# Optimization experiments

Hardware: AMD Instinct MI355X
Metric: run time of the kernel (lower is better)

Reference implementation:

```python
import jax, jax.numpy as jnp
import numpy as np

THRESHOLD = 1e-3  # hardcoded `thresholds = 0.001` in the sparse branch


def setup_inputs() -> dict:
    key = jax.random.key(0)
    k1, k2, k3, k4, k5 = jax.random.split(key, 5)
    b, r, d_in, d_out = 8, 4096, 768, 768
    x = jax.random.normal(k1, (b, r, d_in), dtype=jnp.float32)
    weight = jax.random.normal(k2, (d_out, d_in), dtype=jnp.float32) * 0.02
    bias = jax.random.normal(k3, (d_out,), dtype=jnp.float32) * 0.02
    U = jax.random.normal(k4, (d_in, d_in), dtype=jnp.float32) * (d_in ** -0.5)
    VT = jax.random.normal(k5, (d_out, d_out), dtype=jnp.float32) * (d_out ** -0.5)
    return {"x": x, "weight": weight, "bias": bias, "U": U, "VT": VT}


def reference(x, weight, bias, U, VT):
    # Sparse path (len_grads >= 30) of LinearFunctionSparseGrad.forward.
    # h = x @ U.T, rotated into the gradient basis.  [b, r, c]
    h = jnp.einsum('brc,dc->brd', x, U)
    # Threshold-sparsify: zero entries with |h| <= 0.001.
    h = jnp.where(jnp.abs(h) > THRESHOLD, h, jnp.zeros((), h.dtype))
    # Original: gather nonzero rows/cols, h[rows][:, cols] @ weight.T[cols],
    # then scatter back via I[:, rows] @ res_. Dropped cols are exactly-zero
    # columns and dropped rows are exactly-zero rows, so the math equals a
    # dense matmul on the masked tensor (no [b*r, b*r] identity needed).
    res = jnp.einsum('brc,oc->bro', h, weight)        # h @ weight.T
    res = jnp.einsum('bro,po->brp', res, VT)          # res_ @ VT.T (self.VT=VT_orig.T => VT here)
    return res + bias
```

## Files before the change

### kernel.cpp

```cpp
#include <hip/hip_runtime.h>
#include <hip/hip_bf16.h>

typedef __bf16 bf16_t;
typedef bf16_t bf16x8 __attribute__((ext_vector_type(8)));
typedef bf16_t bf16x4 __attribute__((ext_vector_type(4)));
typedef float  f32x4  __attribute__((ext_vector_type(4)));

#define BM 256
#define BN 256
#define BK 64

enum { EPI_NONE = 0, EPI_THRESH = 1, EPI_BIAS = 2 };

__device__ __forceinline__ void memfence() { asm volatile("" ::: "memory"); }
__device__ __forceinline__ void blockbar() {
    memfence(); __builtin_amdgcn_s_barrier(); memfence();
}

#define GLD16(src, dst) __builtin_amdgcn_global_load_lds( \
    (const __attribute__((address_space(1))) void*)(src), \
    (__attribute__((address_space(3))) void*)(dst), 16, 0, 0)

template <int EPI, typename CT>
__device__ __forceinline__
void gemm_tile(const bf16_t* __restrict__ A, const bf16_t* __restrict__ B,
               CT* __restrict__ C, const float* __restrict__ bias,
               int m0, int n0, int N, int K,
               bf16_t* __restrict__ As, bf16_t* __restrict__ Bs)
{
    const int lane = threadIdx.x & 63;
    const int wave = threadIdx.x >> 6;
    const int wm = wave >> 2;
    const int wn = wave & 3;

    const int fm  = lane & 15;
    const int ql  = lane >> 4;
    const int fsw = fm & 7;

    const int NT = K / BK;

    const int choff = ((lane & 7) ^ ((lane >> 3) & 7)) * 8;
    const bf16_t* pA[2]; const bf16_t* pB[2];
    int sd[2];
#pragma unroll
    for (int l = 0; l < 2; ++l) {
        const int r = (wave * 2 + l) * 8 + (lane >> 3);
        pA[l] = A + (size_t)(m0 + r) * K + choff;
        pB[l] = B + (size_t)(n0 + r) * K + choff;
        sd[l] = (wave * 2 + l) * 64;
    }

#define STAGE_TILE(tt, Ad, Bd) do {                                          \
    _Pragma("unroll") for (int h_ = 0; h_ < 2; ++h_)                         \
    _Pragma("unroll") for (int l_ = 0; l_ < 2; ++l_) {                       \
        GLD16(pA[l_] + (size_t)h_ * 128 * K + (size_t)(tt) * BK,             \
              (Ad) + (size_t)(h_ * 1024 + sd[l_]) * 8);                      \
        GLD16(pB[l_] + (size_t)h_ * 128 * K + (size_t)(tt) * BK,             \
              (Bd) + (size_t)(h_ * 1024 + sd[l_]) * 8);                      \
    } } while (0)

#define LOAD_A(mh) do {                                                      \
    _Pragma("unroll") for (int i_ = 0; i_ < 4; ++i_)                         \
    _Pragma("unroll") for (int k_ = 0; k_ < 2; ++k_)                         \
        af[i_][k_] = *(const bf16x8*)(Ab + (size_t)(                         \
            (wm * 128 + (mh) * 64 + i_ * 16 + fm) * 8 +                      \
            ((k_ * 4 + ql) ^ fsw)) * 8); } while (0)

#define LOAD_B(nh) do {                                                      \
    _Pragma("unroll") for (int j_ = 0; j_ < 2; ++j_)                         \
    _Pragma("unroll") for (int k_ = 0; k_ < 2; ++k_)                         \
        bfx[j_][k_] = *(const bf16x8*)(Bb + (size_t)(                        \
            (wn * 64 + (nh) * 32 + j_ * 16 + fm) * 8 +                       \
            ((k_ * 4 + ql) ^ fsw)) * 8); } while (0)

#define MFMA_Q(mh, nh) do {                                                  \
    _Pragma("unroll") for (int i_ = 0; i_ < 4; ++i_)                         \
    _Pragma("unroll") for (int j_ = 0; j_ < 2; ++j_)                         \
    _Pragma("unroll") for (int k_ = 0; k_ < 2; ++k_)                         \
        acc[(mh) * 4 + i_][(nh) * 2 + j_] =                                  \
            __builtin_amdgcn_mfma_f32_16x16x32_bf16(                         \
                af[i_][k_], bfx[j_][k_],                                     \
                acc[(mh) * 4 + i_][(nh) * 2 + j_], 0, 0, 0); } while (0)

#define PHASE_TAIL(mh, nh) do {                                              \
    blockbar();                                                              \
    asm volatile("s_waitcnt lgkmcnt(0)" ::: "memory");                       \
    __builtin_amdgcn_sched_barrier(0);                                       \
    __builtin_amdgcn_s_setprio(1);                                           \
    MFMA_Q(mh, nh);                                                          \
    __builtin_amdgcn_s_setprio(0);                                           \
    blockbar(); } while (0)

    f32x4 acc[8][4];
#pragma unroll
    for (int i = 0; i < 8; ++i)
#pragma unroll
        for (int j = 0; j < 4; ++j) acc[i][j] = (f32x4){0.f, 0.f, 0.f, 0.f};

    STAGE_TILE(0, As, Bs);
    asm volatile("s_waitcnt vmcnt(0)" ::: "memory");
    blockbar();

    for (int t = 0; t < NT; ++t) {
        const int cur = t & 1;
        const bf16_t* __restrict__ Ab = As + cur * (BM * BK);
        const bf16_t* __restrict__ Bb = Bs + cur * (BN * BK);
        bf16_t* Asd = As + (cur ^ 1) * (BM * BK);
        bf16_t* Bsd = Bs + (cur ^ 1) * (BN * BK);

        bf16x8 af[4][2], bfx[2][2];

        LOAD_A(0); LOAD_B(0);
        if (t + 1 < NT) STAGE_TILE(t + 1, Asd, Bsd);
        PHASE_TAIL(0, 0);

        LOAD_B(1);
        PHASE_TAIL(0, 1);

        LOAD_A(1);
        PHASE_TAIL(1, 1);

        LOAD_B(0);
        asm volatile("s_waitcnt vmcnt(0)" ::: "memory");
        PHASE_TAIL(1, 0);
    }

#pragma unroll
    for (int mi = 0; mi < 8; ++mi) {
#pragma unroll
        for (int ni = 0; ni < 4; ++ni) {
            const int col = n0 + wn * 64 + ni * 16 + fm;
            float bv = 0.f;
            if (EPI == EPI_BIAS) bv = bias[col];
#pragma unroll
            for (int r = 0; r < 4; ++r) {
                const int row = m0 + wm * 128 + mi * 16 + ql * 4 + r;
                float v = acc[mi][ni][r];
                if (EPI == EPI_THRESH) v = (fabsf(v) > 1e-3f) ? v : 0.f;
                if (EPI == EPI_BIAS) v += bv;
                C[(size_t)row * N + col] = (CT)v;
            }
        }
    }

#undef STAGE_TILE
#undef LOAD_A
#undef LOAD_B
#undef MFMA_Q
#undef PHASE_TAIL
}

__global__ __launch_bounds__(512, 2)
void gemm_h_wc(const bf16_t* __restrict__ xb, const bf16_t* __restrict__ Ub,
               bf16_t* __restrict__ h,
               const bf16_t* __restrict__ VTb, const bf16_t* __restrict__ Wt,
               bf16_t* __restrict__ Wc)
{
    __shared__ __align__(16) bf16_t As[2 * BM * BK];
    __shared__ __align__(16) bf16_t Bs[2 * BN * BK];
    const int b = blockIdx.x;
    if (b < 384) {
        const int L = (b & 7) * 48 + (b >> 3);
        gemm_tile<EPI_THRESH, bf16_t>(xb, Ub, h, nullptr,
                                      (L / 3) * BM, (L % 3) * BN, 768, 768, As, Bs);
    } else {
        const int b2 = b - 384;
        gemm_tile<EPI_NONE, bf16_t>(VTb, Wt, Wc, nullptr,
                                    (b2 / 3) * BM, (b2 % 3) * BN, 768, 768, As, Bs);
    }
}

__global__ __launch_bounds__(512, 2)
void gemm_out(const bf16_t* __restrict__ h, const bf16_t* __restrict__ Wc,
              float* __restrict__ out, const float* __restrict__ bias)
{
    __shared__ __align__(16) bf16_t As[2 * BM * BK];
    __shared__ __align__(16) bf16_t Bs[2 * BN * BK];
    const int b = blockIdx.x;
    const int L = (b & 7) * 48 + (b >> 3);
    gemm_tile<EPI_BIAS, float>(h, Wc, out, bias,
                               (L / 3) * BM, (L % 3) * BN, 768, 768, As, Bs);
}

__global__ __launch_bounds__(256)
void prep(const float* __restrict__ x, const float* __restrict__ U,
          const float* __restrict__ VT, const float* __restrict__ w,
          bf16_t* __restrict__ xb, bf16_t* __restrict__ Ub,
          bf16_t* __restrict__ VTb, bf16_t* __restrict__ Wt)
{
    __shared__ float tt[32][33];
    const int b = blockIdx.x;
    if (b < 25728) {
        const float* src; bf16_t* dst; int i;
        if (b < 24576)      { src = x;  dst = xb;  i = b * 256 + threadIdx.x; }
        else if (b < 25152) { src = U;  dst = Ub;  i = (b - 24576) * 256 + threadIdx.x; }
        else                { src = VT; dst = VTb; i = (b - 25152) * 256 + threadIdx.x; }
        const f32x4 v = ((const f32x4*)src)[i];
        bf16x4 o;
        o[0] = (bf16_t)v[0]; o[1] = (bf16_t)v[1];
        o[2] = (bf16_t)v[2]; o[3] = (bf16_t)v[3];
        ((bf16x4*)dst)[i] = o;
    } else {
        const int t = b - 25728;
        const int bx = (t % 24) * 32, by = (t / 24) * 32;
        const int tx = threadIdx.x & 31, ty = threadIdx.x >> 5;
#pragma unroll
        for (int i = 0; i < 32; i += 8)
            tt[ty + i][tx] = w[(size_t)(by + ty + i) * 768 + bx + tx];
        __syncthreads();
#pragma unroll
        for (int i = 0; i < 32; i += 8)
            Wt[(size_t)(bx + ty + i) * 768 + by + tx] = (bf16_t)tt[tx][ty + i];
    }
}

extern "C" void kernel_launch(void* const* d_in, const int* in_sizes, int n_in,
                              void* d_out, int out_size, void* d_ws, size_t ws_size,
                              hipStream_t stream)
{
    const float* x    = (const float*)d_in[0];
    const float* w    = (const float*)d_in[1];
    const float* bias = (const float*)d_in[2];
    const float* U    = (const float*)d_in[3];
    const float* VT   = (const float*)d_in[4];
    float* out = (float*)d_out;

    const int D = 768;
    const int M = 8 * 4096;
    const size_t MD = (size_t)M * D;
    const size_t DD = (size_t)D * D;

    char* ws = (char*)d_ws;
    bf16_t* xb  = (bf16_t*)ws;
    bf16_t* h   = (bf16_t*)(ws + MD * 2);
    bf16_t* Ub  = (bf16_t*)(ws + MD * 4);
    bf16_t* VTb = (bf16_t*)(ws + MD * 4 + DD * 2);
    bf16_t* Wt  = (bf16_t*)(ws + MD * 4 + DD * 4);
    bf16_t* Wc  = (bf16_t*)(ws + MD * 4 + DD * 6);

    prep<<<26304, 256, 0, stream>>>(x, U, VT, w, xb, Ub, VTb, Wt);
    gemm_h_wc<<<384 + 9, 512, 0, stream>>>(xb, Ub, h, VTb, Wt, Wc);
    gemm_out<<<384, 512, 0, stream>>>(h, Wc, out, bias);
}
```

Measured before the change: 299.8 us.

## Fuse fp32-to-bf16 conversion into first GEMM loads, drop prep kernel

Removes the separate prep kernel that converted x, U, VT and transposed W to bf16. The first GEMM now reads fp32 directly through registers, converts to bf16 and writes into swizzled LDS. It uses a new 256x128 tile with double-buffering through registers instead of direct global-to-LDS loads. This avoids writing and re-reading a bf16 copy of x, but it reads fp32 x twice as wide per GEMM pass (once per N tile) and loses the async LDS load path, and the strided W read is uncoalesced.

```diff
diff --git a/kernel.cpp b/kernel.cpp
--- a/kernel.cpp
+++ b/kernel.cpp
@@ -6,8 +6,6 @@
 typedef bf16_t bf16x4 __attribute__((ext_vector_type(4)));
 typedef float  f32x4  __attribute__((ext_vector_type(4)));
 
-#define BM 256
-#define BN 256
 #define BK 64
 
 enum { EPI_NONE = 0, EPI_THRESH = 1, EPI_BIAS = 2 };
@@ -21,12 +19,171 @@
     (const __attribute__((address_space(1))) void*)(src), \
     (__attribute__((address_space(3))) void*)(dst), 16, 0, 0)
 
-template <int EPI, typename CT>
+template <int EPI, int STRIDED_B>
 __device__ __forceinline__
-void gemm_tile(const bf16_t* __restrict__ A, const bf16_t* __restrict__ B,
-               CT* __restrict__ C, const float* __restrict__ bias,
-               int m0, int n0, int N, int K,
-               bf16_t* __restrict__ As, bf16_t* __restrict__ Bs)
+void gemm_h_tile(const float* __restrict__ A, const float* __restrict__ B,
+                 bf16_t* __restrict__ C, int m0, int n0, int N, int K,
+                 bf16_t* __restrict__ As, bf16_t* __restrict__ Bs)
+{
+    const int lane = threadIdx.x & 63;
+    const int wave = threadIdx.x >> 6;
+    const int wm = wave >> 1;
+    const int wn = wave & 1;
+
+    const int fm  = lane & 15;
+    const int ql  = lane >> 4;
+    const int fsw = fm & 7;
+
+    const int NT = K / BK;
+
+    const int arow = wave * 32 + (lane >> 1);
+    const int acb  = (lane & 1) * 4;
+    const float* pa = A + (size_t)(m0 + arow) * K + acb * 8;
+    const int brow = wave * 16 + (lane >> 2);
+    const int bcb  = (lane & 3) * 2;
+    const float* pb = STRIDED_B ? (B + (size_t)(n0 + brow))
+                                : (B + (size_t)(n0 + brow) * K + bcb * 8);
+
+    f32x4 ar[8]; f32x4 brv[4]; float bsv[16];
+
+#define H_ISSUE(tt) do {                                                     \
+    _Pragma("unroll") for (int i_ = 0; i_ < 8; ++i_)                         \
+        ar[i_] = *(const f32x4*)(pa + (size_t)(tt) * BK + i_ * 4);           \
+    if (!STRIDED_B) {                                                        \
+        _Pragma("unroll") for (int i_ = 0; i_ < 4; ++i_)                     \
+            brv[i_] = *(const f32x4*)(pb + (size_t)(tt) * BK + i_ * 4);      \
+    } else {                                                                 \
+        _Pragma("unroll") for (int i_ = 0; i_ < 16; ++i_)                    \
+            bsv[i_] = pb[(size_t)((tt) * BK + bcb * 8 + i_) * K];            \
+    } } while (0)
+
+#define H_WRITE(Ad, Bd) do {                                                 \
+    _Pragma("unroll") for (int c_ = 0; c_ < 4; ++c_) {                       \
+        bf16x8 w_;                                                           \
+        _Pragma("unroll") for (int e_ = 0; e_ < 4; ++e_) {                   \
+            w_[e_]     = (bf16_t)ar[c_ * 2][e_];                             \
+            w_[4 + e_] = (bf16_t)ar[c_ * 2 + 1][e_];                         \
+        }                                                                    \
+        *(bf16x8*)((Ad) + (size_t)(arow * 8 + ((acb + c_) ^ (arow & 7))) * 8)\
+            = w_;                                                            \
+    }                                                                        \
+    _Pragma("unroll") for (int c_ = 0; c_ < 2; ++c_) {                       \
+        bf16x8 w_;                                                           \
+        if (!STRIDED_B) {                                                    \
+            _Pragma("unroll") for (int e_ = 0; e_ < 4; ++e_) {               \
+                w_[e_]     = (bf16_t)brv[c_ * 2][e_];                        \
+                w_[4 + e_] = (bf16_t)brv[c_ * 2 + 1][e_];                    \
+            }                                                                \
+        } else {                                                             \
+            _Pragma("unroll") for (int e_ = 0; e_ < 8; ++e_)                 \
+                w_[e_] = (bf16_t)bsv[c_ * 8 + e_];                           \
+        }                                                                    \
+        *(bf16x8*)((Bd) + (size_t)(brow * 8 + ((bcb + c_) ^ (brow & 7))) * 8)\
+            = w_;                                                            \
+    } } while (0)
+
+    f32x4 acc[4][4];
+#pragma unroll
+    for (int i = 0; i < 4; ++i)
+#pragma unroll
+        for (int j = 0; j < 4; ++j) acc[i][j] = (f32x4){0.f, 0.f, 0.f, 0.f};
+
+    H_ISSUE(0);
+    asm volatile("s_waitcnt vmcnt(0)" ::: "memory");
+    H_WRITE(As, Bs);
+    asm volatile("s_waitcnt lgkmcnt(0)" ::: "memory");
+    blockbar();
+
+    for (int t = 0; t < NT; ++t) {
+        const int cur = t & 1;
+        const bf16_t* __restrict__ Ab = As + cur * (256 * BK);
+        const bf16_t* __restrict__ Bb = Bs + cur * (128 * BK);
+        bf16_t* Asd = As + (cur ^ 1) * (256 * BK);
+        bf16_t* Bsd = Bs + (cur ^ 1) * (128 * BK);
+        const bool stage = (t + 1 < NT);
+
+        bf16x8 af[4][2], bfr[2][2];
+
+        if (stage) H_ISSUE(t + 1);
+#pragma unroll
+        for (int i = 0; i < 4; ++i) {
+            const int row = wm * 64 + i * 16 + fm;
+#pragma unroll
+            for (int kk = 0; kk < 2; ++kk)
+                af[i][kk] = *(const bf16x8*)(Ab + (size_t)(row * 8 + ((kk * 4 + ql) ^ fsw)) * 8);
+        }
+#pragma unroll
+        for (int j = 0; j < 2; ++j) {
+            const int row = wn * 64 + j * 16 + fm;
+#pragma unroll
+            for (int kk = 0; kk < 2; ++kk)
+                bfr[j][kk] = *(const bf16x8*)(Bb + (size_t)(row * 8 + ((kk * 4 + ql) ^ fsw)) * 8);
+        }
+        blockbar();
+        asm volatile("s_waitcnt lgkmcnt(0)" ::: "memory");
+        __builtin_amdgcn_sched_barrier(0);
+        __builtin_amdgcn_s_setprio(1);
+#pragma unroll
+        for (int i = 0; i < 4; ++i)
+#pragma unroll
+            for (int j = 0; j < 2; ++j)
+#pragma unroll
+                for (int kk = 0; kk < 2; ++kk)
+                    acc[i][j] = __builtin_amdgcn_mfma_f32_16x16x32_bf16(
+                        af[i][kk], bfr[j][kk], acc[i][j], 0, 0, 0);
+        __builtin_amdgcn_s_setprio(0);
+        blockbar();
+
+#pragma unroll
+        for (int j = 0; j < 2; ++j) {
+            const int row = wn * 64 + (j + 2) * 16 + fm;
+#pragma unroll
+            for (int kk = 0; kk < 2; ++kk)
+                bfr[j][kk] = *(const bf16x8*)(Bb + (size_t)(row * 8 + ((kk * 4 + ql) ^ fsw)) * 8);
+        }
+        if (stage) {
+            asm volatile("s_waitcnt vmcnt(0)" ::: "memory");
+            H_WRITE(Asd, Bsd);
+        }
+        asm volatile("s_waitcnt lgkmcnt(0)" ::: "memory");
+        blockbar();
+        __builtin_amdgcn_sched_barrier(0);
+        __builtin_amdgcn_s_setprio(1);
+#pragma unroll
+        for (int i = 0; i < 4; ++i)
+#pragma unroll
+            for (int j = 0; j < 2; ++j)
+#pragma unroll
+                for (int kk = 0; kk < 2; ++kk)
+                    acc[i][j + 2] = __builtin_amdgcn_mfma_f32_16x16x32_bf16(
+                        af[i][kk], bfr[j][kk], acc[i][j + 2], 0, 0, 0);
+        __builtin_amdgcn_s_setprio(0);
+        blockbar();
+    }
+
+#pragma unroll
+    for (int i = 0; i < 4; ++i) {
+#pragma unroll
+        for (int j = 0; j < 4; ++j) {
+            const int col = n0 + wn * 64 + j * 16 + fm;
+#pragma unroll
+            for (int r = 0; r < 4; ++r) {
+                const int row = m0 + wm * 64 + i * 16 + ql * 4 + r;
+                float v = acc[i][j][r];
+                if (EPI == EPI_THRESH) v = (fabsf(v) > 1e-3f) ? v : 0.f;
+                C[(size_t)row * N + col] = (bf16_t)v;
+            }
+        }
+    }
+#undef H_ISSUE
+#undef H_WRITE
+}
+
+__device__ __forceinline__
+void gemm_o_tile(const bf16_t* __restrict__ A, const bf16_t* __restrict__ B,
+                 float* __restrict__ C, const float* __restrict__ bias,
+                 int m0, int n0, int N, int K,
+                 bf16_t* __restrict__ As, bf16_t* __restrict__ Bs)
 {
     const int lane = threadIdx.x & 63;
     const int wave = threadIdx.x >> 6;
@@ -103,10 +260,10 @@
 
     for (int t = 0; t < NT; ++t) {
         const int cur = t & 1;
-        const bf16_t* __restrict__ Ab = As + cur * (BM * BK);
-        const bf16_t* __restrict__ Bb = Bs + cur * (BN * BK);
-        bf16_t* Asd = As + (cur ^ 1) * (BM * BK);
-        bf16_t* Bsd = Bs + (cur ^ 1) * (BN * BK);
+        const bf16_t* __restrict__ Ab = As + cur * (256 * BK);
+        const bf16_t* __restrict__ Bb = Bs + cur * (256 * BK);
+        bf16_t* Asd = As + (cur ^ 1) * (256 * BK);
+        bf16_t* Bsd = Bs + (cur ^ 1) * (256 * BK);
 
         bf16x8 af[4][2], bfx[2][2];
 
@@ -130,19 +287,14 @@
 #pragma unroll
         for (int ni = 0; ni < 4; ++ni) {
             const int col = n0 + wn * 64 + ni * 16 + fm;
-            float bv = 0.f;
-            if (EPI == EPI_BIAS) bv = bias[col];
+            const float bv = bias[col];
 #pragma unroll
             for (int r = 0; r < 4; ++r) {
                 const int row = m0 + wm * 128 + mi * 16 + ql * 4 + r;
-                float v = acc[mi][ni][r];
-                if (EPI == EPI_THRESH) v = (fabsf(v) > 1e-3f) ? v : 0.f;
-                if (EPI == EPI_BIAS) v += bv;
-                C[(size_t)row * N + col] = (CT)v;
+                C[(size_t)row * N + col] = acc[mi][ni][r] + bv;
             }
         }
     }
-
 #undef STAGE_TILE
 #undef LOAD_A
 #undef LOAD_B
@@ -151,22 +303,22 @@
 }
 
 __global__ __launch_bounds__(512, 2)
-void gemm_h_wc(const bf16_t* __restrict__ xb, const bf16_t* __restrict__ Ub,
+void gemm_h_wc(const float* __restrict__ x, const float* __restrict__ U,
                bf16_t* __restrict__ h,
-               const bf16_t* __restrict__ VTb, const bf16_t* __restrict__ Wt,
+               const float* __restrict__ VT, const float* __restrict__ w,
                bf16_t* __restrict__ Wc)
 {
-    __shared__ __align__(16) bf16_t As[2 * BM * BK];
-    __shared__ __align__(16) bf16_t Bs[2 * BN * BK];
+    __shared__ __align__(16) bf16_t As[2 * 256 * BK];
+    __shared__ __align__(16) bf16_t Bs[2 * 128 * BK];
     const int b = blockIdx.x;
-    if (b < 384) {
-        const int L = (b & 7) * 48 + (b >> 3);
-        gemm_tile<EPI_THRESH, bf16_t>(xb, Ub, h, nullptr,
-                                      (L / 3) * BM, (L % 3) * BN, 768, 768, As, Bs);
+    if (b < 768) {
+        const int L = (b & 7) * 96 + (b >> 3);
+        gemm_h_tile<EPI_THRESH, 0>(x, U, h,
+                                   (L / 6) * 256, (L % 6) * 128, 768, 768, As, Bs);
     } else {
-        const int b2 = b - 384;
-        gemm_tile<EPI_NONE, bf16_t>(VTb, Wt, Wc, nullptr,
-                                    (b2 / 3) * BM, (b2 % 3) * BN, 768, 768, As, Bs);
+        const int b2 = b - 768;
+        gemm_h_tile<EPI_NONE, 1>(VT, w, Wc,
+                                 (b2 / 6) * 256, (b2 % 6) * 128, 768, 768, As, Bs);
     }
 }
 
@@ -174,44 +326,12 @@
 void gemm_out(const bf16_t* __restrict__ h, const bf16_t* __restrict__ Wc,
               float* __restrict__ out, const float* __restrict__ bias)
 {
-    __shared__ __align__(16) bf16_t As[2 * BM * BK];
-    __shared__ __align__(16) bf16_t Bs[2 * BN * BK];
+    __shared__ __align__(16) bf16_t As[2 * 256 * BK];
+    __shared__ __align__(16) bf16_t Bs[2 * 256 * BK];
     const int b = blockIdx.x;
     const int L = (b & 7) * 48 + (b >> 3);
-    gemm_tile<EPI_BIAS, float>(h, Wc, out, bias,
-                               (L / 3) * BM, (L % 3) * BN, 768, 768, As, Bs);
-}
-
-__global__ __launch_bounds__(256)
-void prep(const float* __restrict__ x, const float* __restrict__ U,
-          const float* __restrict__ VT, const float* __restrict__ w,
-          bf16_t* __restrict__ xb, bf16_t* __restrict__ Ub,
-          bf16_t* __restrict__ VTb, bf16_t* __restrict__ Wt)
-{
-    __shared__ float tt[32][33];
-    const int b = blockIdx.x;
-    if (b < 25728) {
-        const float* src; bf16_t* dst; int i;
-        if (b < 24576)      { src = x;  dst = xb;  i = b * 256 + threadIdx.x; }
-        else if (b < 25152) { src = U;  dst = Ub;  i = (b - 24576) * 256 + threadIdx.x; }
-        else                { src = VT; dst = VTb; i = (b - 25152) * 256 + threadIdx.x; }
-        const f32x4 v = ((const f32x4*)src)[i];
-        bf16x4 o;
-        o[0] = (bf16_t)v[0]; o[1] = (bf16_t)v[1];
-        o[2] = (bf16_t)v[2]; o[3] = (bf16_t)v[3];
-        ((bf16x4*)dst)[i] = o;
-    } else {
-        const int t = b - 25728;
-        const int bx = (t % 24) * 32, by = (t / 24) * 32;
-        const int tx = threadIdx.x & 31, ty = threadIdx.x >> 5;
-#pragma unroll
-        for (int i = 0; i < 32; i += 8)
-            tt[ty + i][tx] = w[(size_t)(by + ty + i) * 768 + bx + tx];
-        __syncthreads();
-#pragma unroll
-        for (int i = 0; i < 32; i += 8)
-            Wt[(size_t)(bx + ty + i) * 768 + by + tx] = (bf16_t)tt[tx][ty + i];
-    }
+    gemm_o_tile(h, Wc, out, bias,
+                (L / 3) * 256, (L % 3) * 256, 768, 768, As, Bs);
 }
 
 extern "C" void kernel_launch(void* const* d_in, const int* in_sizes, int n_in,
@@ -228,17 +348,11 @@
     const int D = 768;
     const int M = 8 * 4096;
     const size_t MD = (size_t)M * D;
-    const size_t DD = (size_t)D * D;
 
     char* ws = (char*)d_ws;
-    bf16_t* xb  = (bf16_t*)ws;
-    bf16_t* h   = (bf16_t*)(ws + MD * 2);
-    bf16_t* Ub  = (bf16_t*)(ws + MD * 4);
-    bf16_t* VTb = (bf16_t*)(ws + MD * 4 + DD * 2);
-    bf16_t* Wt  = (bf16_t*)(ws + MD * 4 + DD * 4);
-    bf16_t* Wc  = (bf16_t*)(ws + MD * 4 + DD * 6);
-
-    prep<<<26304, 256, 0, stream>>>(x, U, VT, w, xb, Ub, VTb, Wt);
-    gemm_h_wc<<<384 + 9, 512, 0, stream>>>(xb, Ub, h, VTb, Wt, Wc);
+    bf16_t* h  = (bf16_t*)ws;
+    bf16_t* Wc = (bf16_t*)(ws + MD * 2);
+
+    gemm_h_wc<<<768 + 18, 512, 0, stream>>>(x, U, h, VT, w, Wc);
     gemm_out<<<384, 512, 0, stream>>>(h, Wc, out, bias);
 }
```

Result: slower. 386.4 us (+28.9%).
